# Kernel tuning notes

Hardware: AMD Instinct MI355X
Metric: run time of the kernel (lower is better)

Reference implementation:

```python
import jax, jax.numpy as jnp
import numpy as np

DIM = 1024
HIDDEN = 2816
NUM_EXPERTS = 8
TOP_K = 2
BATCH, SEQ = 4, 2048


def setup_inputs() -> dict:
    key = jax.random.key(0)
    ks = jax.random.split(key, 5)
    x = jax.random.normal(ks[0], (BATCH, SEQ, DIM), dtype=jnp.float32)
    gate_w = jax.random.normal(ks[1], (NUM_EXPERTS, DIM), dtype=jnp.float32) * 0.02
    w1 = jax.random.normal(ks[2], (NUM_EXPERTS, HIDDEN, DIM), dtype=jnp.float32) * 0.02
    w3 = jax.random.normal(ks[3], (NUM_EXPERTS, HIDDEN, DIM), dtype=jnp.float32) * 0.02
    w2 = jax.random.normal(ks[4], (NUM_EXPERTS, DIM, HIDDEN), dtype=jnp.float32) * 0.02
    return {"x": x, "gate_w": gate_w, "w1": w1, "w3": w3, "w2": w2}


def reference(x, gate_w, w1, w3, w2):
    orig_shape = x.shape
    xf = x.reshape(-1, x.shape[-1])                      # [T, D]
    T = xf.shape[0]
    E, K = gate_w.shape[0], TOP_K

    # gating: softmax over experts, then top-k (descending, matches torch.topk)
    scores = jax.nn.softmax(xf @ gate_w.T, axis=-1)      # [T, E]
    expert_weights, expert_indices = jax.lax.top_k(scores, K)  # [T, K]
    expert_weights = expert_weights / jnp.sum(expert_weights, axis=-1, keepdims=True)

    # dispatch: each token duplicated K times (torch repeat_interleave)
    x_rep = jnp.repeat(xf, K, axis=0)                    # [T*K, D]
    flat_idx = expert_indices.reshape(-1)                # [T*K]

    # per-expert masked SwiGLU FFN, combined into y (loop over small fixed E)
    y = jnp.zeros_like(x_rep)
    for e in range(E):
        m = (flat_idx == e)[:, None]
        xe = jnp.where(m, x_rep, 0.0)                    # zero non-routed tokens
        h = jax.nn.silu(xe @ w1[e].T) * (xe @ w3[e].T)   # [T*K, H]
        out = h @ w2[e].T                                # [T*K, D]
        y = y + jnp.where(m, out, 0.0)

    # weighted combine over the K slots
    y = jnp.sum(y.reshape(T, K, -1) * expert_weights[..., None], axis=1)
    return y.reshape(orig_shape)
```

## Files before the change

### kernel.cpp

```cpp
#include <hip/hip_runtime.h>
#include <hip/hip_bf16.h>

#define NTOK 8192
#define DIM 1024
#define HID 2816
#define NE 8
#define NSLOT (NTOK*2)
#define BM 128
#define BK 32
#define MAXMT (NSLOT/BM + NE)

typedef float f32x4 __attribute__((ext_vector_type(4)));
typedef __bf16 bf16x8 __attribute__((ext_vector_type(8)));
typedef __bf16 bf16x4 __attribute__((ext_vector_type(4)));

#define MFMA(a,b,c) __builtin_amdgcn_mfma_f32_16x16x32_bf16(a,b,c,0,0,0)
#define SWZ(r,g) (((r)<<5) + ((((g) ^ (((r)>>1)&3)))<<3))

__device__ __forceinline__ void cvt_st8(__bf16* d, f32x4 a, f32x4 b){
  bf16x8 v;
  v[0]=(__bf16)a.x; v[1]=(__bf16)a.y; v[2]=(__bf16)a.z; v[3]=(__bf16)a.w;
  v[4]=(__bf16)b.x; v[5]=(__bf16)b.y; v[6]=(__bf16)b.z; v[7]=(__bf16)b.w;
  *reinterpret_cast<bf16x8*>(d) = v;
}
__device__ __forceinline__ void gld_lds16(const void* g, void* l){
  __builtin_amdgcn_global_load_lds(
    (const __attribute__((address_space(1))) void*)g,
    (__attribute__((address_space(3))) void*)l, 16, 0, 0);
}
__device__ __forceinline__ int xcd_map(int orig, int nwg){
  int q = nwg>>3, rr = nwg&7, x = orig&7, o = orig>>3;
  return (x<rr ? x*(q+1) : rr*(q+1)+(x-rr)*q) + o;
}

#define GATEB (NTOK/8)
#define CVTPB (NE*HID*DIM/16/256)
__global__ __launch_bounds__(256) void k_cvtgate(
    const float* __restrict__ x,  const float* __restrict__ gw,
    const float* __restrict__ s1, const float* __restrict__ s3,
    __bf16* __restrict__ d1, __bf16* __restrict__ d3,
    int* __restrict__ idxs, float* __restrict__ wt, __bf16* __restrict__ xb)
{
  int tid = threadIdx.x;
  if(blockIdx.x >= GATEB){
    int cb  = blockIdx.x - GATEB;
    int seg = cb / CVTPB;
    size_t i = (size_t)(cb % CVTPB)*256 + tid;
    const float* src = (seg==0) ? s1 : s3;
    __bf16*      dst = (seg==0) ? d1 : d3;
    const f32x4* s = reinterpret_cast<const f32x4*>(src) + i*4;
    f32x4 a = __builtin_nontemporal_load(s);
    f32x4 b = __builtin_nontemporal_load(s+1);
    f32x4 c = __builtin_nontemporal_load(s+2);
    f32x4 d = __builtin_nontemporal_load(s+3);
    cvt_st8(dst + i*16,     a, b);
    cvt_st8(dst + i*16 + 8, c, d);
    return;
  }

  __shared__ double part[8][8][4];
  __shared__ double lg[8][8];

  int tl = tid>>5, e = (tid>>2)&7, q = tid&3;
  int t  = blockIdx.x*8 + tl;

  const f32x4* x4 = reinterpret_cast<const f32x4*>(x)  + (size_t)t*256 + q*64;
  const f32x4* g4 = reinterpret_cast<const f32x4*>(gw) + e*256 + q*64;

  double s0 = 0.0, s1d = 0.0;
#pragma unroll 4
  for(int j=0;j<64;j+=2){
    f32x4 a0 = x4[j],   b0 = g4[j];
    f32x4 a1 = x4[j+1], b1 = g4[j+1];
    s0  += (double)a0.x*b0.x + (double)a0.y*b0.y
         + (double)a0.z*b0.z + (double)a0.w*b0.w;
    s1d += (double)a1.x*b1.x + (double)a1.y*b1.y
         + (double)a1.z*b1.z + (double)a1.w*b1.w;
  }
  part[tl][e][q] = s0 + s1d;
  __syncthreads();
  if(q==0)
    lg[tl][e] = part[tl][e][0] + part[tl][e][1] + part[tl][e][2] + part[tl][e][3];
  __syncthreads();

  if(tid < 8){
    int tt = blockIdx.x*8 + tid;
    int i1=0; double m1=lg[tid][0];
#pragma unroll
    for(int k=1;k<NE;k++) if(lg[tid][k]>m1){ m1=lg[tid][k]; i1=k; }
    int i2=-1; double m2=-1e300;
#pragma unroll
    for(int k=0;k<NE;k++) if(k!=i1 && lg[tid][k]>m2){ m2=lg[tid][k]; i2=k; }
    float e2 = __expf((float)(m2-m1));
    float w0 = 1.f/(1.f+e2);
    idxs[2*tt]=i1; idxs[2*tt+1]=i2;
    wt[2*tt]=w0;   wt[2*tt+1]=e2*w0;
  }

  const f32x4* xs = reinterpret_cast<const f32x4*>(x) + (size_t)blockIdx.x*2048;
  __bf16* xo = xb + (size_t)blockIdx.x*8192;
#pragma unroll
  for(int k=0;k<4;k++){
    int c = k*256 + tid;
    cvt_st8(xo + (size_t)c*8, xs[2*c], xs[2*c+1]);
  }
}

__global__ __launch_bounds__(256) void k_prep(const int* __restrict__ idxs,
    int* __restrict__ off, int* __restrict__ mtp, int* __restrict__ cursor)
{
  __shared__ int hist[NE];
  int tid = threadIdx.x;
  if(tid < NE) hist[tid] = 0;
  __syncthreads();
  int local[NE] = {0,0,0,0,0,0,0,0};
  for(int k=0;k<NSLOT/256;k++){
    int e = idxs[tid*(NSLOT/256) + k];
    local[e]++;
  }
#pragma unroll
  for(int e=0;e<NE;e++) if(local[e]) atomicAdd(&hist[e], local[e]);
  __syncthreads();
  if(tid==0){
    int o=0, m=0; off[0]=0; mtp[0]=0;
    for(int e=0;e<NE;e++){
      cursor[e]=o; o += hist[e]; off[e+1]=o;
      m += (hist[e]+BM-1)/BM;  mtp[e+1]=m;
    }
  }
}

__global__ __launch_bounds__(256) void k_scatter(const int* __restrict__ idxs,
    int* __restrict__ cursor, int* __restrict__ order, int* __restrict__ inv)
{
  int t = blockIdx.x*blockDim.x + threadIdx.x;
#pragma unroll
  for(int k=0;k<2;k++){
    int s = 2*t+k;
    int e = idxs[s];
    int p = atomicAdd(&cursor[e],1);
    order[p]=s; inv[s]=p;
  }
}

#define FFN1B (MAXMT*(HID/128))
#define CVT2B (NE*DIM*HID/16/512)
__global__ __launch_bounds__(512) void k_ffn1(
    const __bf16* __restrict__ xb, const __bf16* __restrict__ w1b,
    const __bf16* __restrict__ w3b, const int* __restrict__ off,
    const int* __restrict__ mtp, const int* __restrict__ order,
    __bf16* __restrict__ h, const float* __restrict__ w2src,
    __bf16* __restrict__ w2b)
{
  __shared__ __align__(16) __bf16 lA [2][BM*BK];
  __shared__ __align__(16) __bf16 lB1[2][BM*BK];
  __shared__ __align__(16) __bf16 lB3[2][BM*BK];

  int tid = threadIdx.x;
  if(blockIdx.x >= FFN1B){
    size_t i = (size_t)(blockIdx.x - FFN1B)*512 + tid;
    const f32x4* s = reinterpret_cast<const f32x4*>(w2src) + i*4;
    f32x4 a = __builtin_nontemporal_load(s);
    f32x4 b = __builtin_nontemporal_load(s+1);
    f32x4 c = __builtin_nontemporal_load(s+2);
    f32x4 d = __builtin_nontemporal_load(s+3);
    cvt_st8(w2b + i*16,     a, b);
    cvt_st8(w2b + i*16 + 8, c, d);
    return;
  }

  const int NT = HID/128;
  int wg = xcd_map(blockIdx.x, FFN1B);
  int mt = wg / NT, nt = wg % NT;
  if (mt >= mtp[NE]) return;
  int e = 0;
  while (mt >= mtp[e+1]) e++;
  int row0    = off[e] + (mt - mtp[e])*BM;
  int row_end = off[e+1];
  int n0      = nt*128;

  int lane = tid&63;
  int srow = tid>>2;
  int scol = ((tid&3) ^ ((srow>>1)&3))<<3;
  int arow = min(row0 + srow, row_end-1);
  int tok  = order[arow] >> 1;
  const __bf16* gA  = xb  + (size_t)tok*DIM + scol;
  const __bf16* gB1 = w1b + (size_t)e*HID*DIM + (size_t)(n0+srow)*DIM + scol;
  const __bf16* gB3 = w3b + (size_t)e*HID*DIM + (size_t)(n0+srow)*DIM + scol;
  int ldso = (tid>>6)<<9;

  int wm = (tid>>6)>>2, wn = (tid>>6)&3;
  int fr = lane & 15, gq = lane>>4;

  f32x4 acc1[4][2], acc3[4][2];
#pragma unroll
  for(int m=0;m<4;m++)
#pragma unroll
    for(int n=0;n<2;n++){ acc1[m][n]=f32x4{0.f,0.f,0.f,0.f}; acc3[m][n]=f32x4{0.f,0.f,0.f,0.f}; }

  gld_lds16(gA,  &lA [0][ldso]);
  gld_lds16(gB1, &lB1[0][ldso]);
  gld_lds16(gB3, &lB3[0][ldso]);
  __syncthreads();

  const int NK = DIM/BK;
  int buf=0;
  for(int kt=0; kt<NK; kt++){
    if(kt+1<NK){
      gld_lds16(gA  + (kt+1)*BK, &lA [buf^1][ldso]);
      gld_lds16(gB1 + (kt+1)*BK, &lB1[buf^1][ldso]);
      gld_lds16(gB3 + (kt+1)*BK, &lB3[buf^1][ldso]);
    }
    bf16x8 av[4], bv[2], cv[2];
#pragma unroll
    for(int m=0;m<4;m++) av[m]=*reinterpret_cast<const bf16x8*>(&lA[buf][SWZ(wm*64+m*16+fr, gq)]);
#pragma unroll
    for(int n=0;n<2;n++){
      bv[n]=*reinterpret_cast<const bf16x8*>(&lB1[buf][SWZ(wn*32+n*16+fr, gq)]);
      cv[n]=*reinterpret_cast<const bf16x8*>(&lB3[buf][SWZ(wn*32+n*16+fr, gq)]);
    }
#pragma unroll
    for(int m=0;m<4;m++)
#pragma unroll
      for(int n=0;n<2;n++){
        acc1[m][n]=MFMA(av[m],bv[n],acc1[m][n]);
        acc3[m][n]=MFMA(av[m],cv[n],acc3[m][n]);
      }
    __syncthreads();
    buf^=1;
  }

#pragma unroll
  for(int m=0;m<4;m++){
    int rbase = row0 + wm*64 + m*16 + (gq<<2);
#pragma unroll
    for(int r=0;r<4;r++){
      if(rbase+r < row_end){
        __bf16* hp = h + (size_t)(rbase+r)*HID + n0 + wn*32 + fr;
#pragma unroll
        for(int n=0;n<2;n++){
          float u = acc1[m][n][r], v = acc3[m][n][r];
          hp[n*16] = (__bf16)( (u/(1.f+__expf(-u))) * v );
        }
      }
    }
  }
}

__global__ __launch_bounds__(256) void k_ffn2(
    const __bf16* __restrict__ h, const __bf16* __restrict__ w2b,
    const int* __restrict__ off, const int* __restrict__ mtp,
    __bf16* __restrict__ ys)
{
  __shared__ __align__(16) __bf16 lA[2][128*BK];
  __shared__ __align__(16) __bf16 lB[2][128*BK];

  const int NT = DIM/128;
  int wg = xcd_map(blockIdx.x, MAXMT*NT);
  int mt = wg / NT, nt = wg % NT;
  if (mt >= mtp[NE]) return;
  int e = 0;
  while (mt >= mtp[e+1]) e++;
  int row0    = off[e] + (mt - mtp[e])*BM;
  int row_end = off[e+1];
  int n0      = nt*128;

  int tid = threadIdx.x, lane = tid&63, wave = tid>>6;
  int srow = tid>>2;
  int scol = ((tid&3) ^ ((srow>>1)&3))<<3;
  int hr0 = min(row0 + srow,      NSLOT-1);
  int hr1 = min(row0 + srow + 64, NSLOT-1);
  const __bf16* gA0 = h   + (size_t)hr0*HID + scol;
  const __bf16* gA1 = h   + (size_t)hr1*HID + scol;
  const __bf16* gB0 = w2b + (size_t)e*DIM*HID + (size_t)(n0+srow)*HID + scol;
  const __bf16* gB1 = w2b + (size_t)e*DIM*HID + (size_t)(n0+srow+64)*HID + scol;
  int ldso = wave<<9;

  int wm = wave>>1, wn = wave&1;
  int fr = lane&15, gq = lane>>4;

  f32x4 acc[4][4];
#pragma unroll
  for(int m=0;m<4;m++)
#pragma unroll
    for(int n=0;n<4;n++) acc[m][n]=f32x4{0.f,0.f,0.f,0.f};

  gld_lds16(gA0, &lA[0][ldso]);
  gld_lds16(gA1, &lA[0][2048+ldso]);
  gld_lds16(gB0, &lB[0][ldso]);
  gld_lds16(gB1, &lB[0][2048+ldso]);
  __syncthreads();

  const int NK = HID/BK;
  int buf=0;
  for(int kt=0; kt<NK; kt++){
    if(kt+1<NK){
      gld_lds16(gA0 + (kt+1)*BK, &lA[buf^1][ldso]);
      gld_lds16(gA1 + (kt+1)*BK, &lA[buf^1][2048+ldso]);
      gld_lds16(gB0 + (kt+1)*BK, &lB[buf^1][ldso]);
      gld_lds16(gB1 + (kt+1)*BK, &lB[buf^1][2048+ldso]);
    }
    bf16x8 av[4], bv[4];
#pragma unroll
    for(int m=0;m<4;m++) av[m]=*reinterpret_cast<const bf16x8*>(&lA[buf][SWZ(wm*64+m*16+fr, gq)]);
#pragma unroll
    for(int n=0;n<4;n++) bv[n]=*reinterpret_cast<const bf16x8*>(&lB[buf][SWZ(wn*64+n*16+fr, gq)]);
#pragma unroll
    for(int m=0;m<4;m++)
#pragma unroll
      for(int n=0;n<4;n++)
        acc[m][n]=MFMA(av[m],bv[n],acc[m][n]);
    __syncthreads();
    buf^=1;
  }

#pragma unroll
  for(int m=0;m<4;m++){
    int rbase = row0 + wm*64 + m*16 + (gq<<2);
#pragma unroll
    for(int r=0;r<4;r++){
      if(rbase+r < row_end){
        __bf16* yp = ys + (size_t)(rbase+r)*DIM + n0 + wn*64 + fr;
#pragma unroll
        for(int n=0;n<4;n++) yp[n*16] = (__bf16)acc[m][n][r];
      }
    }
  }
}

__global__ __launch_bounds__(256) void k_combine(
    const __bf16* __restrict__ ys, const int* __restrict__ inv,
    const float* __restrict__ wt, float* __restrict__ y)
{
  int t  = blockIdx.x;
  int p0 = inv[2*t], p1 = inv[2*t+1];
  float w0 = wt[2*t], w1v = wt[2*t+1];
  int d = threadIdx.x*4;
  const __bf16* r0 = ys + (size_t)p0*DIM + d;
  const __bf16* r1 = ys + (size_t)p1*DIM + d;
  f32x4 o;
#pragma unroll
  for(int j=0;j<4;j++) o[j] = w0*(float)r0[j] + w1v*(float)r1[j];
  *reinterpret_cast<f32x4*>(y + (size_t)t*DIM + d) = o;
}

extern "C" void kernel_launch(void* const* d_in, const int* in_sizes, int n_in,
                              void* d_out, int out_size, void* d_ws, size_t ws_size,
                              hipStream_t stream)
{
  const float* x  = (const float*)d_in[0];
  const float* gw = (const float*)d_in[1];
  const float* w1 = (const float*)d_in[2];
  const float* w3 = (const float*)d_in[3];
  const float* w2 = (const float*)d_in[4];
  float* y = (float*)d_out;
  char* ws = (char*)d_ws;

  int*   off    = (int*)(ws + 64);
  int*   mtp    = (int*)(ws + 128);
  int*   cursor = (int*)(ws + 256);
  int*   idxs   = (int*)(ws + 320);
  float* wt     = (float*)(ws + 320 + 65536);
  int*   order  = (int*)(ws + 320 + 2*65536);
  int*   inv    = (int*)(ws + 320 + 3*65536);
  __bf16* h     = (__bf16*)(ws + 262464);
  __bf16* xb    = (__bf16*)(ws + 262464 + 92274688ull);
  __bf16* w1b   = (__bf16*)(ws + 262464 + 92274688ull + 16777216ull);
  __bf16* w3b   = (__bf16*)(ws + 262464 + 92274688ull + 16777216ull + 46137344ull);
  __bf16* w2b   = (__bf16*)(ws + 262464 + 92274688ull + 16777216ull + 2*46137344ull);
  __bf16* ysb   = w1b;

  k_cvtgate<<<GATEB + 2*CVTPB, 256, 0, stream>>>(x, gw, w1, w3,
                                                 w1b, w3b, idxs, wt, xb);
  k_prep   <<<1, 256, 0, stream>>>(idxs, off, mtp, cursor);
  k_scatter<<<NTOK/256, 256, 0, stream>>>(idxs, cursor, order, inv);
  k_ffn1   <<<FFN1B + CVT2B, 512, 0, stream>>>(xb, w1b, w3b, off, mtp, order,
                                               h, w2, w2b);
  k_ffn2   <<<MAXMT*(DIM/128), 256, 0, stream>>>(h, w2b, off, mtp, ysb);
  k_combine<<<NTOK, 256, 0, stream>>>(ysb, inv, wt, y);
}
```

Before: 615.1 us.

## Enlarge FFN2 tiles to 256x256 with 8-wave ping-pong pipelined MFMA schedule

Rewrites the down-projection GEMM to use 256x256 output tiles with BK=64, 512 threads, and a hand-scheduled multi-phase loop. The loop interleaves async global-to-LDS loads with MFMA bursts, using explicit vmcnt waits, barriers, sched_barrier and setprio. The aim is higher arithmetic intensity per tile and better overlap of memory and compute. In exchange, padding waste per expert grows with the bigger M tile, fewer workgroups are launched (MAXMT2*4), and it adds a second tile-prefix array in the prep kernel.

Measured after the change: 642.5 us. +4.5%, slower.

```diff
diff --git a/kernel.cpp b/kernel.cpp
--- a/kernel.cpp
+++ b/kernel.cpp
@@ -9,6 +9,9 @@
 #define BM 128
 #define BK 32
 #define MAXMT (NSLOT/BM + NE)
+#define BM2 256
+#define BK2 64
+#define MAXMT2 (NSLOT/BM2 + NE)
 
 typedef float f32x4 __attribute__((ext_vector_type(4)));
 typedef __bf16 bf16x8 __attribute__((ext_vector_type(8)));
@@ -16,6 +19,8 @@
 
 #define MFMA(a,b,c) __builtin_amdgcn_mfma_f32_16x16x32_bf16(a,b,c,0,0,0)
 #define SWZ(r,g) (((r)<<5) + ((((g) ^ (((r)>>1)&3)))<<3))
+#define VMW(N) asm volatile("s_waitcnt vmcnt(" #N ")" ::: "memory")
+#define NOP do{}while(0)
 
 __device__ __forceinline__ void cvt_st8(__bf16* d, f32x4 a, f32x4 b){
   bf16x8 v;
@@ -107,7 +112,8 @@
 }
 
 __global__ __launch_bounds__(256) void k_prep(const int* __restrict__ idxs,
-    int* __restrict__ off, int* __restrict__ mtp, int* __restrict__ cursor)
+    int* __restrict__ off, int* __restrict__ mtp, int* __restrict__ mtp2,
+    int* __restrict__ cursor)
 {
   __shared__ int hist[NE];
   int tid = threadIdx.x;
@@ -122,10 +128,11 @@
   for(int e=0;e<NE;e++) if(local[e]) atomicAdd(&hist[e], local[e]);
   __syncthreads();
   if(tid==0){
-    int o=0, m=0; off[0]=0; mtp[0]=0;
+    int o=0, m=0, m2=0; off[0]=0; mtp[0]=0; mtp2[0]=0;
     for(int e=0;e<NE;e++){
       cursor[e]=o; o += hist[e]; off[e+1]=o;
-      m += (hist[e]+BM-1)/BM;  mtp[e+1]=m;
+      m  += (hist[e]+BM-1)>>7;   mtp[e+1]=m;
+      m2 += (hist[e]+BM2-1)>>8;  mtp2[e+1]=m2;
     }
   }
 }
@@ -247,76 +254,102 @@
   }
 }
 
-__global__ __launch_bounds__(256) void k_ffn2(
+#define LIDX(buf, rb, kk) (((((buf)*2 + (rb))*2 + (kk))<<12))
+__global__ __launch_bounds__(512) void k_ffn2(
     const __bf16* __restrict__ h, const __bf16* __restrict__ w2b,
-    const int* __restrict__ off, const int* __restrict__ mtp,
+    const int* __restrict__ off, const int* __restrict__ mtp2,
     __bf16* __restrict__ ys)
 {
-  __shared__ __align__(16) __bf16 lA[2][128*BK];
-  __shared__ __align__(16) __bf16 lB[2][128*BK];
-
-  const int NT = DIM/128;
-  int wg = xcd_map(blockIdx.x, MAXMT*NT);
+  __shared__ __align__(16) __bf16 lA[2*2*2*4096];
+  __shared__ __align__(16) __bf16 lB[2*2*2*4096];
+
+  const int NT = DIM/256;
+  int wg = xcd_map(blockIdx.x, MAXMT2*NT);
   int mt = wg / NT, nt = wg % NT;
-  if (mt >= mtp[NE]) return;
+  if (mt >= mtp2[NE]) return;
   int e = 0;
-  while (mt >= mtp[e+1]) e++;
-  int row0    = off[e] + (mt - mtp[e])*BM;
+  while (mt >= mtp2[e+1]) e++;
+  int row0    = off[e] + (mt - mtp2[e])*BM2;
   int row_end = off[e+1];
-  int n0      = nt*128;
+  int n0      = nt*256;
 
   int tid = threadIdx.x, lane = tid&63, wave = tid>>6;
-  int srow = tid>>2;
-  int scol = ((tid&3) ^ ((srow>>1)&3))<<3;
-  int hr0 = min(row0 + srow,      NSLOT-1);
-  int hr1 = min(row0 + srow + 64, NSLOT-1);
+  int wm = wave>>2, wn = wave&3;
+  int fr = lane&15, gq = lane>>4;
+
+  int sr = tid>>2, gloc = tid&3;
+  int scol = ((gloc ^ ((sr>>1)&3))<<3);
+  int hr0 = min(row0 + sr,       NSLOT-1);
+  int hr1 = min(row0 + 128 + sr, NSLOT-1);
   const __bf16* gA0 = h   + (size_t)hr0*HID + scol;
   const __bf16* gA1 = h   + (size_t)hr1*HID + scol;
-  const __bf16* gB0 = w2b + (size_t)e*DIM*HID + (size_t)(n0+srow)*HID + scol;
-  const __bf16* gB1 = w2b + (size_t)e*DIM*HID + (size_t)(n0+srow+64)*HID + scol;
+  const __bf16* gB0 = w2b + (size_t)e*DIM*HID + (size_t)(n0+sr)*HID + scol;
+  const __bf16* gB1 = w2b + (size_t)e*DIM*HID + (size_t)(n0+128+sr)*HID + scol;
   int ldso = wave<<9;
 
-  int wm = wave>>1, wn = wave&1;
-  int fr = lane&15, gq = lane>>4;
-
-  f32x4 acc[4][4];
-#pragma unroll
-  for(int m=0;m<4;m++)
+  f32x4 acc[8][4];
+#pragma unroll
+  for(int m=0;m<8;m++)
 #pragma unroll
     for(int n=0;n<4;n++) acc[m][n]=f32x4{0.f,0.f,0.f,0.f};
 
-  gld_lds16(gA0, &lA[0][ldso]);
-  gld_lds16(gA1, &lA[0][2048+ldso]);
-  gld_lds16(gB0, &lB[0][ldso]);
-  gld_lds16(gB1, &lB[0][2048+ldso]);
-  __syncthreads();
-
-  const int NK = HID/BK;
-  int buf=0;
-  for(int kt=0; kt<NK; kt++){
-    if(kt+1<NK){
-      gld_lds16(gA0 + (kt+1)*BK, &lA[buf^1][ldso]);
-      gld_lds16(gA1 + (kt+1)*BK, &lA[buf^1][2048+ldso]);
-      gld_lds16(gB0 + (kt+1)*BK, &lB[buf^1][ldso]);
-      gld_lds16(gB1 + (kt+1)*BK, &lB[buf^1][2048+ldso]);
-    }
-    bf16x8 av[4], bv[4];
-#pragma unroll
-    for(int m=0;m<4;m++) av[m]=*reinterpret_cast<const bf16x8*>(&lA[buf][SWZ(wm*64+m*16+fr, gq)]);
-#pragma unroll
-    for(int n=0;n<4;n++) bv[n]=*reinterpret_cast<const bf16x8*>(&lB[buf][SWZ(wn*64+n*16+fr, gq)]);
-#pragma unroll
-    for(int m=0;m<4;m++)
-#pragma unroll
-      for(int n=0;n<4;n++)
-        acc[m][n]=MFMA(av[m],bv[n],acc[m][n]);
-    __syncthreads();
-    buf^=1;
-  }
-
-#pragma unroll
-  for(int m=0;m<4;m++){
-    int rbase = row0 + wm*64 + m*16 + (gq<<2);
+#define STG_A(buf, kk, kt_) { \
+    gld_lds16(gA0 + (size_t)(kt_)*BK2 + (kk)*32, &lA[LIDX(buf,0,kk)+ldso]); \
+    gld_lds16(gA1 + (size_t)(kt_)*BK2 + (kk)*32, &lA[LIDX(buf,1,kk)+ldso]); }
+#define STG_B(buf, kk, kt_) { \
+    gld_lds16(gB0 + (size_t)(kt_)*BK2 + (kk)*32, &lB[LIDX(buf,0,kk)+ldso]); \
+    gld_lds16(gB1 + (size_t)(kt_)*BK2 + (kk)*32, &lB[LIDX(buf,1,kk)+ldso]); }
+
+#define PH(buf, kk, mh, RB, STAGE, WAITC) { \
+    bf16x8 av[4]; \
+    _Pragma("unroll") for(int m_=0;m_<4;m_++) \
+      av[m_] = *(const bf16x8*)&lA[LIDX(buf,wm,kk) + SWZ(((mh)*4+m_)*16 + fr, gq)]; \
+    if(RB){ _Pragma("unroll") for(int n_=0;n_<4;n_++) \
+      bv[n_] = *(const bf16x8*)&lB[LIDX(buf,(wn>>1),kk) + SWZ((wn&1)*64 + n_*16 + fr, gq)]; } \
+    STAGE; \
+    __builtin_amdgcn_s_barrier(); \
+    asm volatile("s_waitcnt lgkmcnt(0)" ::: "memory"); \
+    __builtin_amdgcn_sched_barrier(0); \
+    __builtin_amdgcn_s_setprio(1); \
+    _Pragma("unroll") for(int m_=0;m_<4;m_++) _Pragma("unroll") for(int n_=0;n_<4;n_++) \
+      acc[(mh)*4+m_][n_] = MFMA(av[m_], bv[n_], acc[(mh)*4+m_][n_]); \
+    __builtin_amdgcn_s_setprio(0); \
+    WAITC; \
+    __builtin_amdgcn_s_barrier(); }
+
+  STG_A(0,0,0); STG_B(0,0,0); STG_A(0,1,0); STG_B(0,1,0);
+  STG_A(1,0,1); STG_B(1,0,1);
+  VMW(8);
+  __builtin_amdgcn_s_barrier();
+
+  bf16x8 bv[4];
+  int kt = 0;
+  const int NTI = (HID/BK2)/2;
+  for(int it=0; it<NTI-1; ++it, kt+=2){
+    PH(0,0,0, 1, STG_A(1,1,kt+1), NOP);
+    PH(0,0,1, 0, STG_B(1,1,kt+1), VMW(8));
+    PH(0,1,0, 1, STG_A(0,0,kt+2), NOP);
+    PH(0,1,1, 0, STG_B(0,0,kt+2), VMW(8));
+    PH(1,0,0, 1, STG_A(0,1,kt+2), NOP);
+    PH(1,0,1, 0, STG_B(0,1,kt+2), VMW(8));
+    PH(1,1,0, 1, STG_A(1,0,kt+3), NOP);
+    PH(1,1,1, 0, STG_B(1,0,kt+3), VMW(8));
+  }
+  PH(0,0,0, 1, STG_A(1,1,kt+1), NOP);
+  PH(0,0,1, 0, STG_B(1,1,kt+1), VMW(8));
+  PH(0,1,0, 1, NOP, NOP);
+  PH(0,1,1, 0, NOP, VMW(4));
+  PH(1,0,0, 1, NOP, NOP);
+  PH(1,0,1, 0, NOP, VMW(0));
+  PH(1,1,0, 1, NOP, NOP);
+  PH(1,1,1, 0, NOP, NOP);
+#undef STG_A
+#undef STG_B
+#undef PH
+
+#pragma unroll
+  for(int m=0;m<8;m++){
+    int rbase = row0 + wm*128 + m*16 + (gq<<2);
 #pragma unroll
     for(int r=0;r<4;r++){
       if(rbase+r < row_end){
@@ -358,6 +391,7 @@
 
   int*   off    = (int*)(ws + 64);
   int*   mtp    = (int*)(ws + 128);
+  int*   mtp2   = (int*)(ws + 192);
   int*   cursor = (int*)(ws + 256);
   int*   idxs   = (int*)(ws + 320);
   float* wt     = (float*)(ws + 320 + 65536);
@@ -372,10 +406,10 @@
 
   k_cvtgate<<<GATEB + 2*CVTPB, 256, 0, stream>>>(x, gw, w1, w3,
                                                  w1b, w3b, idxs, wt, xb);
-  k_prep   <<<1, 256, 0, stream>>>(idxs, off, mtp, cursor);
+  k_prep   <<<1, 256, 0, stream>>>(idxs, off, mtp, mtp2, cursor);
   k_scatter<<<NTOK/256, 256, 0, stream>>>(idxs, cursor, order, inv);
   k_ffn1   <<<FFN1B + CVT2B, 512, 0, stream>>>(xb, w1b, w3b, off, mtp, order,
                                                h, w2, w2b);
-  k_ffn2   <<<MAXMT*(DIM/128), 256, 0, stream>>>(h, w2b, off, mtp, ysb);
+  k_ffn2   <<<MAXMT2*(DIM/256), 512, 0, stream>>>(h, w2b, off, mtp2, ysb);
   k_combine<<<NTOK, 256, 0, stream>>>(ysb, inv, wt, y);
 }
```
